# Kernel tuning notes

Hardware: AMD Instinct MI355X
Metric: run time of the kernel (lower is better)

## Reference

```python
import jax, jax.numpy as jnp
import numpy as np

B, CW_DIM, Z_DIM = 512, 4096, 1024
DIM_CODES, BOOK_SIZE, DIM_EMBED = 64, 1024, 64
ENC_H, DEC_H = 512, 2048
SLOPE = 0.2  # LeakyReLU negative slope

def lrelu(v):
    return jnp.where(v > 0, v, SLOPE * v)

def setup_inputs() -> dict:
    key = jax.random.key(0)
    ks = jax.random.split(key, 12)
    s = 0.02
    inp = {
        'x': jax.random.normal(ks[0], (B, CW_DIM), jnp.float32),
        'codebook': jax.random.normal(ks[1], (DIM_CODES, BOOK_SIZE, DIM_EMBED), jnp.float32),
        'enc_w1': jax.random.normal(ks[2], (ENC_H, DIM_EMBED), jnp.float32) * s,
        'enc_b1': jnp.zeros((ENC_H,), jnp.float32),
        'enc_w2': jax.random.normal(ks[3], (2 * Z_DIM, ENC_H), jnp.float32) * s,
        'enc_b2': jnp.zeros((2 * Z_DIM,), jnp.float32),
        'inf1_w': jax.random.normal(ks[4], (Z_DIM // 2, 2 * Z_DIM), jnp.float32) * s,
        'inf1_b': jnp.zeros((Z_DIM // 2,), jnp.float32),
        'inf2_w1': jax.random.normal(ks[5], (2 * Z_DIM, 9 * Z_DIM // 4), jnp.float32) * s,
        'inf2_b1': jnp.zeros((2 * Z_DIM,), jnp.float32),
        'inf2_w2': jax.random.normal(ks[6], (3 * Z_DIM // 2, 2 * Z_DIM), jnp.float32) * s,
        'inf2_b2': jnp.zeros((3 * Z_DIM // 2,), jnp.float32),
        'prior_w1': jax.random.normal(ks[7], (2 * Z_DIM, Z_DIM // 4), jnp.float32) * s,
        'prior_b1': jnp.zeros((2 * Z_DIM,), jnp.float32),
        'prior_w2': jax.random.normal(ks[8], (3 * Z_DIM // 2, 2 * Z_DIM), jnp.float32) * s,
        'prior_b2': jnp.zeros((3 * Z_DIM // 2,), jnp.float32),
        'dec_w1': jax.random.normal(ks[9], (DEC_H, 3 * Z_DIM // 4), jnp.float32) * s,
        'dec_b1': jnp.zeros((DEC_H,), jnp.float32),
        'dec_w2': jax.random.normal(ks[10], (CW_DIM, DEC_H), jnp.float32) * s,
        'dec_b2': jnp.zeros((CW_DIM,), jnp.float32),
    }
    return inp

def reference(x, codebook, enc_w1, enc_b1, enc_w2, enc_b2,
              inf1_w, inf1_b, inf2_w1, inf2_b1, inf2_w2, inf2_b2,
              prior_w1, prior_b1, prior_w2, prior_b2,
              dec_w1, dec_b1, dec_w2, dec_b2):
    b = x.shape[0]
    # ---- encode: view (B, dim_codes, dim_embed), per-code conv + max-pool + Linear
    xe = x.reshape(b, DIM_CODES, DIM_EMBED)                       # (B, C, E)
    feat = lrelu(jnp.einsum('bce,he->bch', xe, enc_w1) + enc_b1)  # (B, C, H)
    h = jnp.max(feat, axis=1) @ enc_w2.T + enc_b2                 # (B, 2z)
    mu, log_var = jnp.split(h @ inf1_w.T + inf1_b, 2, axis=1)     # (B, z/4) each
    z1 = mu                                                        # eval mode: sample == mu
    # ---- decode
    p = lrelu(z1 @ prior_w1.T + prior_b1) @ prior_w2.T + prior_b2
    p_mu, p_logvar = jnp.split(p, 2, axis=1)                       # (B, 3z/4) each
    d = lrelu(jnp.concatenate([z1, h], axis=1) @ inf2_w1.T + inf2_b1) @ inf2_w2.T + inf2_b2
    d_mu, d_log_var = jnp.split(d, 2, axis=1)
    z2 = d_mu + p_mu                                               # eval mode sample
    cw_recon = lrelu(z2 @ dec_w1.T + dec_b1) @ dec_w2.T + dec_b2   # (B, cw_dim)
    # ---- dist: squared distance to (detached) codebook, no explicit repeat
    xr = cw_recon.reshape(b, DIM_CODES, DIM_EMBED)
    book = jax.lax.stop_gradient(codebook)                         # (C, S, E)
    cw_dist = ((xr ** 2).sum(-1)[..., None]
               + (book ** 2).sum(-1)[None]
               - 2.0 * jnp.einsum('bce,cse->bcs', xr, book))       # (B, C, S)
    idx = jnp.argmin(cw_dist, axis=-1).reshape(b * DIM_CODES, 1)   # matches torch (B*C, 1)
    return (cw_recon, cw_dist, idx, mu, log_var, d_mu, d_log_var, p_logvar)
```

## Files before the change

### kernel.cpp

```cpp
#include <hip/hip_runtime.h>
#include <hip/hip_bf16.h>

typedef __hip_bfloat16 bf16;
typedef unsigned short u16;

#define BATCH 512
#define CW_DIM 4096
#define DIM_CODES 64
#define BOOK_SIZE 1024
#define DIM_EMBED 64
#define ENC_H 512

__device__ __forceinline__ float bf2f(u16 u) {
    unsigned int x = ((unsigned int)u) << 16;
    return __uint_as_float(x);
}
__device__ __forceinline__ float loadf(const void* p, size_t i, int bf) {
    if (bf) return bf2f(((const u16*)p)[i]);
    return ((const float*)p)[i];
}
__device__ __forceinline__ double loadd(const void* p, size_t i, int bf) {
    return (double)loadf(p, i, bf);
}
__device__ __forceinline__ float4 load4(const void* p, size_t i, int bf) {
    if (bf) {
        const u16* q = (const u16*)p + i;
        uint2 raw = *reinterpret_cast<const uint2*>(q);
        float4 r;
        r.x = bf2f((u16)(raw.x & 0xFFFF));
        r.y = bf2f((u16)(raw.x >> 16));
        r.z = bf2f((u16)(raw.y & 0xFFFF));
        r.w = bf2f((u16)(raw.y >> 16));
        return r;
    }
    return *reinterpret_cast<const float4*>((const float*)p + i);
}
__device__ __forceinline__ void stored(void* p, size_t i, int bf, double v) {
    if (bf) ((bf16*)p)[i] = __float2bfloat16((float)v);
    else    ((float*)p)[i] = (float)v;
}
__device__ __forceinline__ u16 f2bfu(float v) {
    bf16 b = __float2bfloat16(v);
    return *reinterpret_cast<u16*>(&b);
}

__global__ void detect_kernel(const u16* __restrict__ x, int* __restrict__ flag) {
    __shared__ int hits;
    if (threadIdx.x == 0) hits = 0;
    __syncthreads();
    int h = 0;
    for (int i = threadIdx.x; i < 16384; i += 256) {
        u16 v = x[2 * i];
        if (((v >> 7) & 0xFF) == 0xFF) h++;
    }
    atomicAdd(&hits, h);
    __syncthreads();
    if (threadIdx.x == 0) *flag = (hits == 0) ? 1 : 0;
}

__global__ void booknorm_kernel(const void* __restrict__ book, double* __restrict__ bn,
                                const int* __restrict__ dflag) {
    const int bf = *dflag;
    int r = blockIdx.x * blockDim.x + threadIdx.x;
    if (r >= DIM_CODES * BOOK_SIZE) return;
    double acc = 0.0;
    for (int e = 0; e < DIM_EMBED; e += 4) {
        float4 v = load4(book, (size_t)r * DIM_EMBED + e, bf);
        acc = fma((double)v.x, (double)v.x, acc);
        acc = fma((double)v.y, (double)v.y, acc);
        acc = fma((double)v.z, (double)v.z, acc);
        acc = fma((double)v.w, (double)v.w, acc);
    }
    bn[r] = acc;
}

__global__ __launch_bounds__(256) void enc_kernel(const void* __restrict__ x,
                                                  const void* __restrict__ w1,
                                                  const void* __restrict__ b1,
                                                  float* __restrict__ hmax,
                                                  const int* __restrict__ dflag) {
    const int bf = *dflag;
    __shared__ float xs_t[64][68];
    __shared__ float wsh_t[64][68];
    __shared__ float red[64][17];
    int t = threadIdx.x;
    int h0 = blockIdx.x * 64;
    int b = blockIdx.y;

    int cr = t >> 2;
    int e0 = (t & 3) << 4;
    for (int q = 0; q < 4; q++) {
        int e = e0 + (q << 2);
        float4 xv = load4(x, (size_t)b * CW_DIM + cr * DIM_EMBED + e, bf);
        xs_t[e + 0][cr] = xv.x; xs_t[e + 1][cr] = xv.y;
        xs_t[e + 2][cr] = xv.z; xs_t[e + 3][cr] = xv.w;
        float4 wv = load4(w1, (size_t)(h0 + cr) * DIM_EMBED + e, bf);
        wsh_t[e + 0][cr] = wv.x; wsh_t[e + 1][cr] = wv.y;
        wsh_t[e + 2][cr] = wv.z; wsh_t[e + 3][cr] = wv.w;
    }
    __syncthreads();

    int th = t & 15, tc = t >> 4;
    float acc[4][4] = {};
    for (int e = 0; e < 64; e++) {
        float4 a4 = *(const float4*)&xs_t[e][tc << 2];
        float4 w4 = *(const float4*)&wsh_t[e][th << 2];
        float aa[4] = {a4.x, a4.y, a4.z, a4.w};
        float ww[4] = {w4.x, w4.y, w4.z, w4.w};
#pragma unroll
        for (int i = 0; i < 4; i++)
#pragma unroll
            for (int j = 0; j < 4; j++)
                acc[i][j] = fmaf(aa[i], ww[j], acc[i][j]);
    }
#pragma unroll
    for (int j = 0; j < 4; j++) {
        float bj = loadf(b1, h0 + (th << 2) + j, bf);
        float m = -1e30f;
#pragma unroll
        for (int i = 0; i < 4; i++) {
            float v = acc[i][j] + bj;
            v = v > 0.f ? v : 0.2f * v;
            m = fmaxf(m, v);
        }
        red[(th << 2) + j][tc] = m;
    }
    __syncthreads();
    if (t < 64) {
        float m = red[t][0];
        for (int k = 1; k < 16; k++) m = fmaxf(m, red[t][k]);
        hmax[(size_t)b * ENC_H + h0 + t] = m;
    }
}

__global__ __launch_bounds__(256) void gemm_kernel(const float* __restrict__ A1, int lda1, int K1,
                                                   const float* __restrict__ A2, int lda2, int Ktot,
                                                   const void* __restrict__ W,
                                                   const void* __restrict__ bias,
                                                   float* __restrict__ C, int N, int act,
                                                   const int* __restrict__ dflag) {
    const int bf = *dflag;
    __shared__ float As[16][68];
    __shared__ float Ws[16][68];
    int t = threadIdx.x;
    int tx = t & 15, ty = t >> 4;
    int n0 = blockIdx.x * 64, m0 = blockIdx.y * 64;
    int mrow = t >> 2, kq = (t & 3) << 2;
    float acc[4][4] = {};
    for (int kt = 0; kt < Ktot; kt += 16) {
        int k = kt + kq;
        float4 av;
        if (k < K1) av = *reinterpret_cast<const float4*>(A1 + (size_t)(m0 + mrow) * lda1 + k);
        else        av = *reinterpret_cast<const float4*>(A2 + (size_t)(m0 + mrow) * lda2 + (k - K1));
        float4 wv = load4(W, (size_t)(n0 + mrow) * Ktot + k, bf);
        As[kq + 0][mrow] = av.x; As[kq + 1][mrow] = av.y;
        As[kq + 2][mrow] = av.z; As[kq + 3][mrow] = av.w;
        Ws[kq + 0][mrow] = wv.x; Ws[kq + 1][mrow] = wv.y;
        Ws[kq + 2][mrow] = wv.z; Ws[kq + 3][mrow] = wv.w;
        __syncthreads();
#pragma unroll
        for (int kk = 0; kk < 16; kk++) {
            float4 a4 = *(const float4*)&As[kk][ty << 2];
            float4 w4 = *(const float4*)&Ws[kk][tx << 2];
            float a[4] = {a4.x, a4.y, a4.z, a4.w};
            float w[4] = {w4.x, w4.y, w4.z, w4.w};
#pragma unroll
            for (int i = 0; i < 4; i++)
#pragma unroll
                for (int j = 0; j < 4; j++)
                    acc[i][j] = fmaf(a[i], w[j], acc[i][j]);
        }
        __syncthreads();
    }
#pragma unroll
    for (int i = 0; i < 4; i++) {
        int m = m0 + (ty << 2) + i;
        float ov[4];
#pragma unroll
        for (int j = 0; j < 4; j++) {
            int n = n0 + (tx << 2) + j;
            float v = acc[i][j] + loadf(bias, n, bf);
            if (act) v = v > 0.f ? v : 0.2f * v;
            ov[j] = v;
        }
        float4 o = {ov[0], ov[1], ov[2], ov[3]};
        *reinterpret_cast<float4*>(C + (size_t)m * N + n0 + (tx << 2)) = o;
    }
}

__global__ void add_kernel(const float* __restrict__ a, int lda_a,
                           const float* __restrict__ b, int lda_b,
                           float* __restrict__ o, int ncolq, int total4) {
    int g = blockIdx.x * blockDim.x + threadIdx.x;
    if (g >= total4) return;
    int m = g / ncolq, j = (g % ncolq) << 2;
    float4 va = *reinterpret_cast<const float4*>(a + (size_t)m * lda_a + j);
    float4 vb = *reinterpret_cast<const float4*>(b + (size_t)m * lda_b + j);
    float4 vo = {va.x + vb.x, va.y + vb.y, va.z + vb.z, va.w + vb.w};
    *reinterpret_cast<float4*>(o + (size_t)g * 4) = vo;
}

__global__ void cast_kernel(const float* __restrict__ src, int lda, int col0, int ncolq,
                            void* __restrict__ out, size_t obase, int total4,
                            const int* __restrict__ dflag) {
    const int bf = *dflag;
    int g = blockIdx.x * blockDim.x + threadIdx.x;
    if (g >= total4) return;
    int m = g / ncolq, j = (g % ncolq) << 2;
    float4 v = *reinterpret_cast<const float4*>(src + (size_t)m * lda + col0 + j);
    if (bf) {
        ushort4 h;
        h.x = f2bfu(v.x); h.y = f2bfu(v.y); h.z = f2bfu(v.z); h.w = f2bfu(v.w);
        *reinterpret_cast<ushort4*>((u16*)out + obase + (size_t)g * 4) = h;
    } else {
        *reinterpret_cast<float4*>((float*)out + obase + (size_t)g * 4) = v;
    }
}

__global__ __launch_bounds__(256, 4) void dist_kernel(const float* __restrict__ cwr,
                                                      const void* __restrict__ book,
                                                      const double* __restrict__ bn,
                                                      void* __restrict__ out,
                                                      size_t odist, size_t oidx,
                                                      const int* __restrict__ dflag) {
    const int bf = *dflag;
    __shared__ double xs[32][64];
    __shared__ double xn[32];
    __shared__ float bs[64][66];
    int t = threadIdx.x;
    int c = blockIdx.x;
    int b0 = blockIdx.y * 32;
    int sl = t & 63, wv = t >> 6;

    for (int i = t; i < 32 * 64; i += 256) {
        int bl = i >> 6, e = i & 63;
        xs[bl][e] = (double)cwr[(size_t)(b0 + bl) * CW_DIM + c * DIM_EMBED + e];
    }
    __syncthreads();
    if (t < 32) {
        double a = 0.0;
        for (int e = 0; e < 64; e++) a = fma(xs[t][e], xs[t][e], a);
        xn[t] = a;
    }

    double bd[8];
    int bsx[8];
#pragma unroll
    for (int p = 0; p < 8; p++) { bd[p] = 1e300; bsx[p] = 0; }

#pragma unroll 1
    for (int st = 0; st < 16; st++) {
        int s0 = st * 64;
        __syncthreads();
#pragma unroll
        for (int i4 = t; i4 < 1024; i4 += 256) {
            int srow = i4 >> 4, e4 = (i4 & 15) << 2;
            float4 v = load4(book, ((size_t)c * BOOK_SIZE + s0 + srow) * DIM_EMBED + e4, bf);
            bs[srow][e4 + 0] = v.x; bs[srow][e4 + 1] = v.y;
            bs[srow][e4 + 2] = v.z; bs[srow][e4 + 3] = v.w;
        }
        __syncthreads();
        double bnv = bn[(size_t)c * BOOK_SIZE + s0 + sl];
#pragma unroll
        for (int pb = 0; pb < 2; pb++) {
            int blb = wv * 8 + pb * 4;
            double a0 = 0.0, a1 = 0.0, a2 = 0.0, a3 = 0.0;
#pragma unroll 8
            for (int e = 0; e < 64; e += 2) {
                float2 bv = *(const float2*)&bs[sl][e];
                double bv0 = (double)bv.x, bv1 = (double)bv.y;
                double2 x0 = *(const double2*)&xs[blb + 0][e];
                double2 x1 = *(const double2*)&xs[blb + 1][e];
                double2 x2 = *(const double2*)&xs[blb + 2][e];
                double2 x3 = *(const double2*)&xs[blb + 3][e];
                a0 = fma(x0.x, bv0, a0); a0 = fma(x0.y, bv1, a0);
                a1 = fma(x1.x, bv0, a1); a1 = fma(x1.y, bv1, a1);
                a2 = fma(x2.x, bv0, a2); a2 = fma(x2.y, bv1, a2);
                a3 = fma(x3.x, bv0, a3); a3 = fma(x3.y, bv1, a3);
            }
            double dv[4];
            dv[0] = a0; dv[1] = a1; dv[2] = a2; dv[3] = a3;
#pragma unroll
            for (int j = 0; j < 4; j++) {
                int bl = blb + j;
                double d = xn[bl] + bnv - 2.0 * dv[j];
                stored(out, odist + ((size_t)(b0 + bl) * DIM_CODES + c) * BOOK_SIZE + s0 + sl, bf, d);
                if (d < bd[pb * 4 + j]) { bd[pb * 4 + j] = d; bsx[pb * 4 + j] = s0 + sl; }
            }
        }
    }
#pragma unroll
    for (int p = 0; p < 8; p++) {
        double d = bd[p];
        int s = bsx[p];
        for (int off = 32; off >= 1; off >>= 1) {
            double od = __shfl_xor(d, off, 64);
            int os = __shfl_xor(s, off, 64);
            if (od < d || (od == d && os < s)) { d = od; s = os; }
        }
        if (sl == 0)
            stored(out, oidx + (size_t)(b0 + wv * 8 + p) * DIM_CODES + c, bf, (double)s);
    }
}

extern "C" void kernel_launch(void* const* d_in, const int* in_sizes, int n_in,
                              void* d_out, int out_size, void* d_ws, size_t ws_size,
                              hipStream_t stream) {
    const void* x        = d_in[0];
    const void* codebook = d_in[1];
    const void* enc_w1   = d_in[2];
    const void* enc_b1   = d_in[3];
    const void* enc_w2   = d_in[4];
    const void* enc_b2   = d_in[5];
    const void* inf1_w   = d_in[6];
    const void* inf1_b   = d_in[7];
    const void* inf2_w1  = d_in[8];
    const void* inf2_b1  = d_in[9];
    const void* inf2_w2  = d_in[10];
    const void* inf2_b2  = d_in[11];
    const void* prior_w1 = d_in[12];
    const void* prior_b1 = d_in[13];
    const void* prior_w2 = d_in[14];
    const void* prior_b2 = d_in[15];
    const void* dec_w1   = d_in[16];
    const void* dec_b1   = d_in[17];
    const void* dec_w2   = d_in[18];
    const void* dec_b2   = d_in[19];

    float* W0 = (float*)d_ws;
    float* inf1out = W0;
    float* pfull   = inf1out + 262144;
    float* dfull   = pfull + 786432;
    float* cwr     = dfull + 786432;
    float* bufA    = cwr + 2097152;
    float* bufB    = bufA + 1048576;
    float* bufC    = bufB + 1048576;
    double* bn     = (double*)(bufC + 393216);
    int* dflag     = (int*)(bn + 65536);

    const size_t o_cwrecon = 0;
    const size_t o_cwdist  = 2097152;
    const size_t o_idx     = 35651584;
    const size_t o_mu      = 35684352;
    const size_t o_logvar  = 35815424;
    const size_t o_dmu     = 35946496;
    const size_t o_dlogvar = 36339712;
    const size_t o_plogvar = 36732928;

    detect_kernel<<<1, 256, 0, stream>>>((const u16*)x, dflag);
    booknorm_kernel<<<256, 256, 0, stream>>>(codebook, bn, dflag);
    enc_kernel<<<dim3(8, BATCH), 256, 0, stream>>>(x, enc_w1, enc_b1, bufC, dflag);

    gemm_kernel<<<dim3(32, 8), 256, 0, stream>>>(bufC, 512, 512, bufC, 512, 512,
                                                 enc_w2, enc_b2, bufA, 2048, 0, dflag);
    gemm_kernel<<<dim3(8, 8), 256, 0, stream>>>(bufA, 2048, 2048, bufA, 2048, 2048,
                                                inf1_w, inf1_b, inf1out, 512, 0, dflag);
    gemm_kernel<<<dim3(32, 8), 256, 0, stream>>>(inf1out, 512, 256, inf1out, 512, 256,
                                                 prior_w1, prior_b1, bufB, 2048, 1, dflag);
    gemm_kernel<<<dim3(24, 8), 256, 0, stream>>>(bufB, 2048, 2048, bufB, 2048, 2048,
                                                 prior_w2, prior_b2, pfull, 1536, 0, dflag);
    gemm_kernel<<<dim3(32, 8), 256, 0, stream>>>(inf1out, 512, 256, bufA, 2048, 2304,
                                                 inf2_w1, inf2_b1, bufB, 2048, 1, dflag);
    gemm_kernel<<<dim3(24, 8), 256, 0, stream>>>(bufB, 2048, 2048, bufB, 2048, 2048,
                                                 inf2_w2, inf2_b2, dfull, 1536, 0, dflag);
    add_kernel<<<384, 256, 0, stream>>>(dfull, 1536, pfull, 1536, bufC, 192, 98304);
    gemm_kernel<<<dim3(32, 8), 256, 0, stream>>>(bufC, 768, 768, bufC, 768, 768,
                                                 dec_w1, dec_b1, bufA, 2048, 1, dflag);
    gemm_kernel<<<dim3(64, 8), 256, 0, stream>>>(bufA, 2048, 2048, bufA, 2048, 2048,
                                                 dec_w2, dec_b2, cwr, 4096, 0, dflag);

    dist_kernel<<<dim3(64, 16), 256, 0, stream>>>(cwr, codebook, bn,
                                                  d_out, o_cwdist, o_idx, dflag);

    cast_kernel<<<2048, 256, 0, stream>>>(cwr, 4096, 0, 1024, d_out, o_cwrecon, 524288, dflag);
    cast_kernel<<<128, 256, 0, stream>>>(inf1out, 512, 0, 64, d_out, o_mu, 32768, dflag);
    cast_kernel<<<128, 256, 0, stream>>>(inf1out, 512, 256, 64, d_out, o_logvar, 32768, dflag);
    cast_kernel<<<384, 256, 0, stream>>>(dfull, 1536, 0, 192, d_out, o_dmu, 98304, dflag);
    cast_kernel<<<384, 256, 0, stream>>>(dfull, 1536, 768, 192, d_out, o_dlogvar, 98304, dflag);
    cast_kernel<<<384, 256, 0, stream>>>(pfull, 1536, 768, 192, d_out, o_plogvar, 98304, dflag);
}
```

Baseline: 1.181 ms.

## Fuse output casts and residual add into GEMM epilogue, enlarge M tile to 128

The GEMM kernel now uses 128x64 tiles with 8x4 register blocking per thread, halving the row-block count. The elementwise add of d_mu and p_mu is folded into the dec_w1 GEMM's A-operand load. The six separate cast kernels are removed by writing the required output slices directly from the GEMM epilogue. This cuts seven kernel launches and the extra memory passes they made, at the cost of fewer blocks per GEMM (lower occupancy on small layers) and more registers.

```diff
diff --git a/kernel.cpp b/kernel.cpp
--- a/kernel.cpp
+++ b/kernel.cpp
@@ -18,9 +18,6 @@
 __device__ __forceinline__ float loadf(const void* p, size_t i, int bf) {
     if (bf) return bf2f(((const u16*)p)[i]);
     return ((const float*)p)[i];
-}
-__device__ __forceinline__ double loadd(const void* p, size_t i, int bf) {
-    return (double)loadf(p, i, bf);
 }
 __device__ __forceinline__ float4 load4(const void* p, size_t i, int bf) {
     if (bf) {
@@ -135,85 +132,93 @@
 
 __global__ __launch_bounds__(256) void gemm_kernel(const float* __restrict__ A1, int lda1, int K1,
                                                    const float* __restrict__ A2, int lda2, int Ktot,
+                                                   const float* __restrict__ Aadd,
                                                    const void* __restrict__ W,
                                                    const void* __restrict__ bias,
                                                    float* __restrict__ C, int N, int act,
+                                                   void* __restrict__ out,
+                                                   size_t s0base, int s0c0, int s0c1, int s0stride,
+                                                   size_t s1base, int s1c0, int s1c1, int s1stride,
                                                    const int* __restrict__ dflag) {
     const int bf = *dflag;
-    __shared__ float As[16][68];
-    __shared__ float Ws[16][68];
+    __shared__ float As[16][136];
+    __shared__ float Ws[16][72];
     int t = threadIdx.x;
     int tx = t & 15, ty = t >> 4;
-    int n0 = blockIdx.x * 64, m0 = blockIdx.y * 64;
-    int mrow = t >> 2, kq = (t & 3) << 2;
-    float acc[4][4] = {};
+    int n0 = blockIdx.x * 64, m0 = blockIdx.y * 128;
+    int arow = t & 127, ak = (t >> 7) * 8;
+    int wrow = t & 63,  wk = (t >> 6) * 4;
+    float acc[8][4] = {};
+#pragma unroll 1
     for (int kt = 0; kt < Ktot; kt += 16) {
-        int k = kt + kq;
-        float4 av;
-        if (k < K1) av = *reinterpret_cast<const float4*>(A1 + (size_t)(m0 + mrow) * lda1 + k);
-        else        av = *reinterpret_cast<const float4*>(A2 + (size_t)(m0 + mrow) * lda2 + (k - K1));
-        float4 wv = load4(W, (size_t)(n0 + mrow) * Ktot + k, bf);
-        As[kq + 0][mrow] = av.x; As[kq + 1][mrow] = av.y;
-        As[kq + 2][mrow] = av.z; As[kq + 3][mrow] = av.w;
-        Ws[kq + 0][mrow] = wv.x; Ws[kq + 1][mrow] = wv.y;
-        Ws[kq + 2][mrow] = wv.z; Ws[kq + 3][mrow] = wv.w;
+#pragma unroll
+        for (int q = 0; q < 2; q++) {
+            int k = kt + ak + q * 4;
+            float4 av;
+            if (k < K1) {
+                av = *reinterpret_cast<const float4*>(A1 + (size_t)(m0 + arow) * lda1 + k);
+                if (Aadd) {
+                    float4 ad = *reinterpret_cast<const float4*>(Aadd + (size_t)(m0 + arow) * lda1 + k);
+                    av.x += ad.x; av.y += ad.y; av.z += ad.z; av.w += ad.w;
+                }
+            } else {
+                av = *reinterpret_cast<const float4*>(A2 + (size_t)(m0 + arow) * lda2 + (k - K1));
+            }
+            As[ak + q * 4 + 0][arow] = av.x; As[ak + q * 4 + 1][arow] = av.y;
+            As[ak + q * 4 + 2][arow] = av.z; As[ak + q * 4 + 3][arow] = av.w;
+        }
+        float4 wv = load4(W, (size_t)(n0 + wrow) * Ktot + kt + wk, bf);
+        Ws[wk + 0][wrow] = wv.x; Ws[wk + 1][wrow] = wv.y;
+        Ws[wk + 2][wrow] = wv.z; Ws[wk + 3][wrow] = wv.w;
         __syncthreads();
 #pragma unroll
         for (int kk = 0; kk < 16; kk++) {
-            float4 a4 = *(const float4*)&As[kk][ty << 2];
-            float4 w4 = *(const float4*)&Ws[kk][tx << 2];
-            float a[4] = {a4.x, a4.y, a4.z, a4.w};
+            float4 a0 = *(const float4*)&As[kk][ty * 8];
+            float4 a1 = *(const float4*)&As[kk][ty * 8 + 4];
+            float4 w4 = *(const float4*)&Ws[kk][tx * 4];
+            float a[8] = {a0.x, a0.y, a0.z, a0.w, a1.x, a1.y, a1.z, a1.w};
             float w[4] = {w4.x, w4.y, w4.z, w4.w};
 #pragma unroll
-            for (int i = 0; i < 4; i++)
+            for (int i = 0; i < 8; i++)
 #pragma unroll
                 for (int j = 0; j < 4; j++)
                     acc[i][j] = fmaf(a[i], w[j], acc[i][j]);
         }
         __syncthreads();
     }
-#pragma unroll
-    for (int i = 0; i < 4; i++) {
-        int m = m0 + (ty << 2) + i;
+    int nbase = n0 + tx * 4;
+    float b0 = loadf(bias, nbase + 0, bf), b1v = loadf(bias, nbase + 1, bf);
+    float b2 = loadf(bias, nbase + 2, bf), b3 = loadf(bias, nbase + 3, bf);
+#pragma unroll
+    for (int i = 0; i < 8; i++) {
+        int m = m0 + ty * 8 + i;
         float ov[4];
-#pragma unroll
-        for (int j = 0; j < 4; j++) {
-            int n = n0 + (tx << 2) + j;
-            float v = acc[i][j] + loadf(bias, n, bf);
-            if (act) v = v > 0.f ? v : 0.2f * v;
-            ov[j] = v;
+        ov[0] = acc[i][0] + b0; ov[1] = acc[i][1] + b1v;
+        ov[2] = acc[i][2] + b2; ov[3] = acc[i][3] + b3;
+        if (act) {
+#pragma unroll
+            for (int j = 0; j < 4; j++) ov[j] = ov[j] > 0.f ? ov[j] : 0.2f * ov[j];
         }
         float4 o = {ov[0], ov[1], ov[2], ov[3]};
-        *reinterpret_cast<float4*>(C + (size_t)m * N + n0 + (tx << 2)) = o;
-    }
-}
-
-__global__ void add_kernel(const float* __restrict__ a, int lda_a,
-                           const float* __restrict__ b, int lda_b,
-                           float* __restrict__ o, int ncolq, int total4) {
-    int g = blockIdx.x * blockDim.x + threadIdx.x;
-    if (g >= total4) return;
-    int m = g / ncolq, j = (g % ncolq) << 2;
-    float4 va = *reinterpret_cast<const float4*>(a + (size_t)m * lda_a + j);
-    float4 vb = *reinterpret_cast<const float4*>(b + (size_t)m * lda_b + j);
-    float4 vo = {va.x + vb.x, va.y + vb.y, va.z + vb.z, va.w + vb.w};
-    *reinterpret_cast<float4*>(o + (size_t)g * 4) = vo;
-}
-
-__global__ void cast_kernel(const float* __restrict__ src, int lda, int col0, int ncolq,
-                            void* __restrict__ out, size_t obase, int total4,
-                            const int* __restrict__ dflag) {
-    const int bf = *dflag;
-    int g = blockIdx.x * blockDim.x + threadIdx.x;
-    if (g >= total4) return;
-    int m = g / ncolq, j = (g % ncolq) << 2;
-    float4 v = *reinterpret_cast<const float4*>(src + (size_t)m * lda + col0 + j);
-    if (bf) {
-        ushort4 h;
-        h.x = f2bfu(v.x); h.y = f2bfu(v.y); h.z = f2bfu(v.z); h.w = f2bfu(v.w);
-        *reinterpret_cast<ushort4*>((u16*)out + obase + (size_t)g * 4) = h;
-    } else {
-        *reinterpret_cast<float4*>((float*)out + obase + (size_t)g * 4) = v;
+        *reinterpret_cast<float4*>(C + (size_t)m * N + nbase) = o;
+        if (nbase >= s0c0 && nbase < s0c1) {
+            size_t off = s0base + (size_t)m * s0stride + (nbase - s0c0);
+            if (bf) {
+                ushort4 h = {f2bfu(ov[0]), f2bfu(ov[1]), f2bfu(ov[2]), f2bfu(ov[3])};
+                *reinterpret_cast<ushort4*>((u16*)out + off) = h;
+            } else {
+                *reinterpret_cast<float4*>((float*)out + off) = o;
+            }
+        }
+        if (nbase >= s1c0 && nbase < s1c1) {
+            size_t off = s1base + (size_t)m * s1stride + (nbase - s1c0);
+            if (bf) {
+                ushort4 h = {f2bfu(ov[0]), f2bfu(ov[1]), f2bfu(ov[2]), f2bfu(ov[3])};
+                *reinterpret_cast<ushort4*>((u16*)out + off) = h;
+            } else {
+                *reinterpret_cast<float4*>((float*)out + off) = o;
+            }
+        }
     }
 }
 
@@ -351,31 +356,35 @@
     booknorm_kernel<<<256, 256, 0, stream>>>(codebook, bn, dflag);
     enc_kernel<<<dim3(8, BATCH), 256, 0, stream>>>(x, enc_w1, enc_b1, bufC, dflag);
 
-    gemm_kernel<<<dim3(32, 8), 256, 0, stream>>>(bufC, 512, 512, bufC, 512, 512,
-                                                 enc_w2, enc_b2, bufA, 2048, 0, dflag);
-    gemm_kernel<<<dim3(8, 8), 256, 0, stream>>>(bufA, 2048, 2048, bufA, 2048, 2048,
-                                                inf1_w, inf1_b, inf1out, 512, 0, dflag);
-    gemm_kernel<<<dim3(32, 8), 256, 0, stream>>>(inf1out, 512, 256, inf1out, 512, 256,
-                                                 prior_w1, prior_b1, bufB, 2048, 1, dflag);
-    gemm_kernel<<<dim3(24, 8), 256, 0, stream>>>(bufB, 2048, 2048, bufB, 2048, 2048,
-                                                 prior_w2, prior_b2, pfull, 1536, 0, dflag);
-    gemm_kernel<<<dim3(32, 8), 256, 0, stream>>>(inf1out, 512, 256, bufA, 2048, 2304,
-                                                 inf2_w1, inf2_b1, bufB, 2048, 1, dflag);
-    gemm_kernel<<<dim3(24, 8), 256, 0, stream>>>(bufB, 2048, 2048, bufB, 2048, 2048,
-                                                 inf2_w2, inf2_b2, dfull, 1536, 0, dflag);
-    add_kernel<<<384, 256, 0, stream>>>(dfull, 1536, pfull, 1536, bufC, 192, 98304);
-    gemm_kernel<<<dim3(32, 8), 256, 0, stream>>>(bufC, 768, 768, bufC, 768, 768,
-                                                 dec_w1, dec_b1, bufA, 2048, 1, dflag);
-    gemm_kernel<<<dim3(64, 8), 256, 0, stream>>>(bufA, 2048, 2048, bufA, 2048, 2048,
-                                                 dec_w2, dec_b2, cwr, 4096, 0, dflag);
+    gemm_kernel<<<dim3(32, 4), 256, 0, stream>>>(bufC, 512, 512, bufC, 512, 512, nullptr,
+                                                 enc_w2, enc_b2, bufA, 2048, 0,
+                                                 d_out, 0, 0, 0, 0, 0, 0, 0, 0, dflag);
+    gemm_kernel<<<dim3(8, 4), 256, 0, stream>>>(bufA, 2048, 2048, bufA, 2048, 2048, nullptr,
+                                                inf1_w, inf1_b, inf1out, 512, 0,
+                                                d_out, o_mu, 0, 256, 256,
+                                                o_logvar, 256, 512, 256, dflag);
+    gemm_kernel<<<dim3(32, 4), 256, 0, stream>>>(inf1out, 512, 256, inf1out, 512, 256, nullptr,
+                                                 prior_w1, prior_b1, bufB, 2048, 1,
+                                                 d_out, 0, 0, 0, 0, 0, 0, 0, 0, dflag);
+    gemm_kernel<<<dim3(24, 4), 256, 0, stream>>>(bufB, 2048, 2048, bufB, 2048, 2048, nullptr,
+                                                 prior_w2, prior_b2, pfull, 1536, 0,
+                                                 d_out, o_plogvar, 768, 1536, 768,
+                                                 0, 0, 0, 0, dflag);
+    gemm_kernel<<<dim3(32, 4), 256, 0, stream>>>(inf1out, 512, 256, bufA, 2048, 2304, nullptr,
+                                                 inf2_w1, inf2_b1, bufB, 2048, 1,
+                                                 d_out, 0, 0, 0, 0, 0, 0, 0, 0, dflag);
+    gemm_kernel<<<dim3(24, 4), 256, 0, stream>>>(bufB, 2048, 2048, bufB, 2048, 2048, nullptr,
+                                                 inf2_w2, inf2_b2, dfull, 1536, 0,
+                                                 d_out, o_dmu, 0, 768, 768,
+                                                 o_dlogvar, 768, 1536, 768, dflag);
+    gemm_kernel<<<dim3(32, 4), 256, 0, stream>>>(dfull, 1536, 768, dfull, 1536, 768, pfull,
+                                                 dec_w1, dec_b1, bufA, 2048, 1,
+                                                 d_out, 0, 0, 0, 0, 0, 0, 0, 0, dflag);
+    gemm_kernel<<<dim3(64, 4), 256, 0, stream>>>(bufA, 2048, 2048, bufA, 2048, 2048, nullptr,
+                                                 dec_w2, dec_b2, cwr, 4096, 0,
+                                                 d_out, o_cwrecon, 0, 4096, 4096,
+                                                 0, 0, 0, 0, dflag);
 
     dist_kernel<<<dim3(64, 16), 256, 0, stream>>>(cwr, codebook, bn,
                                                   d_out, o_cwdist, o_idx, dflag);
-
-    cast_kernel<<<2048, 256, 0, stream>>>(cwr, 4096, 0, 1024, d_out, o_cwrecon, 524288, dflag);
-    cast_kernel<<<128, 256, 0, stream>>>(inf1out, 512, 0, 64, d_out, o_mu, 32768, dflag);
-    cast_kernel<<<128, 256, 0, stream>>>(inf1out, 512, 256, 64, d_out, o_logvar, 32768, dflag);
-    cast_kernel<<<384, 256, 0, stream>>>(dfull, 1536, 0, 192, d_out, o_dmu, 98304, dflag);
-    cast_kernel<<<384, 256, 0, stream>>>(dfull, 1536, 768, 192, d_out, o_dlogvar, 98304, dflag);
-    cast_kernel<<<384, 256, 0, stream>>>(pfull, 1536, 768, 192, d_out, o_plogvar, 98304, dflag);
-}
+}
```

Measured after the change: 1.788 ms. 1.51x slower.
